# Kernel tuning notes

Measured on AMD Instinct MI355X. Metric: run time of the kernel, lower is better.

Reference implementation:

```python
import jax, jax.numpy as jnp
import numpy as np

EPS = 1e-10

def _mlp(x, W1, b1, W2, b2):
    # Linear -> ReLU -> Linear (matches _MultiLayerPercep)
    return jnp.maximum(x @ W1 + b1, 0.0) @ W2 + b2

def setup_inputs() -> dict:
    key = jax.random.key(0)
    ks = jax.random.split(key, 24)
    B, P, Q, P2, D = 512, 100, 40, 40, 64
    Nu, Ni, Nr = 100000, 100000, 6

    def lin(k, fi, fo):
        kw, kb = jax.random.split(k)
        s = 1.0 / np.sqrt(fi)
        return (jax.random.uniform(kw, (fi, fo), jnp.float32, -s, s),
                jax.random.uniform(kb, (fo,), jnp.float32, -s, s))

    uids = jax.random.randint(ks[0], (B,), 0, Nu)
    u_item_pad = jnp.stack([jax.random.randint(ks[1], (B, P), 0, Ni),
                            jax.random.randint(ks[2], (B, P), 0, Nr)], axis=-1)
    u_user_pad = jax.random.randint(ks[3], (B, Q), 0, Nu)
    u_user_item_pad = jnp.stack([jax.random.randint(ks[4], (B, Q, P2), 0, Ni),
                                 jax.random.randint(ks[5], (B, Q, P2), 0, Nr)], axis=-1)

    user_table = jax.random.normal(ks[6], (Nu, D), jnp.float32) * 0.1
    item_table = jax.random.normal(ks[7], (Ni, D), jnp.float32) * 0.1
    rate_table = jax.random.normal(ks[8], (Nr, D), jnp.float32) * 0.1

    gv_W1, gv_b1 = lin(ks[9], 2 * D, D)
    gv_W2, gv_b2 = lin(ks[10], D, D)
    atti_W1, atti_b1 = lin(ks[11], 2 * D, D)
    atti_W2, atti_b2 = lin(ks[12], D, 1)
    agg_W, agg_b = lin(ks[13], D, D)
    attu_W1, attu_b1 = lin(ks[14], 2 * D, D)
    attu_W2, attu_b2 = lin(ks[15], D, 1)
    aggn_W, aggn_b = lin(ks[16], D, D)
    cm_W1, cm_b1 = lin(ks[17], 2 * D, D)
    cm_W2, cm_b2 = lin(ks[18], D, D)
    cm_W3, cm_b3 = lin(ks[19], D, D)

    return dict(uids=uids, u_item_pad=u_item_pad, u_user_pad=u_user_pad,
                u_user_item_pad=u_user_item_pad,
                user_table=user_table, item_table=item_table, rate_table=rate_table,
                gv_W1=gv_W1, gv_b1=gv_b1, gv_W2=gv_W2, gv_b2=gv_b2,
                atti_W1=atti_W1, atti_b1=atti_b1, atti_W2=atti_W2, atti_b2=atti_b2,
                agg_W=agg_W, agg_b=agg_b,
                attu_W1=attu_W1, attu_b1=attu_b1, attu_W2=attu_W2, attu_b2=attu_b2,
                aggn_W=aggn_W, aggn_b=aggn_b,
                cm_W1=cm_W1, cm_b1=cm_b1, cm_W2=cm_W2, cm_b2=cm_b2, cm_W3=cm_W3, cm_b3=cm_b3)

def reference(uids, u_item_pad, u_user_pad, u_user_item_pad,
              user_table, item_table, rate_table,
              gv_W1, gv_b1, gv_W2, gv_b2,
              atti_W1, atti_b1, atti_W2, atti_b2,
              agg_W, agg_b,
              attu_W1, attu_b1, attu_W2, attu_b2,
              aggn_W, aggn_b,
              cm_W1, cm_b1, cm_W2, cm_b2, cm_W3, cm_b3):
    f32 = jnp.float32

    # ---- item aggregation branch ----
    q_a = item_table[u_item_pad[:, :, 0]]                      # [B,P,D]
    mask_u = (u_item_pad[:, :, 0] > 0).astype(f32)             # [B,P]
    er = rate_table[u_item_pad[:, :, 1]]                       # [B,P,D]
    x_ia = _mlp(jnp.concatenate([q_a, er], -1), gv_W1, gv_b1, gv_W2, gv_b2)
    p_i = mask_u[..., None] * user_table[uids][:, None, :]     # [B,P,D]
    alpha = _mlp(jnp.concatenate([x_ia, p_i], -1), atti_W1, atti_b1, atti_W2, atti_b2)[..., 0]
    alpha = jnp.exp(alpha) * mask_u
    alpha = alpha / (jnp.sum(alpha, axis=1, keepdims=True) + EPS)
    h_iI = jnp.maximum(jnp.sum(alpha[..., None] * x_ia, axis=1) @ agg_W + agg_b, 0.0)  # [B,D]

    # ---- social branch: per-neighbor item aggregation ----
    q_a_s = item_table[u_user_item_pad[:, :, :, 0]]            # [B,Q,P2,D]
    mask_s = (u_user_item_pad[:, :, :, 0] > 0).astype(f32)     # [B,Q,P2]
    er_s = rate_table[u_user_item_pad[:, :, :, 1]]
    x_ia_s = _mlp(jnp.concatenate([q_a_s, er_s], -1), gv_W1, gv_b1, gv_W2, gv_b2)
    nbr_emb = user_table[u_user_pad]                           # [B,Q,D]
    p_i_s = mask_s[..., None] * nbr_emb[:, :, None, :]
    alpha_s = _mlp(jnp.concatenate([x_ia_s, p_i_s], -1), atti_W1, atti_b1, atti_W2, atti_b2)[..., 0]
    alpha_s = jnp.exp(alpha_s) * mask_s
    alpha_s = alpha_s / (jnp.sum(alpha_s, axis=2, keepdims=True) + EPS)
    h_oI = jnp.maximum(jnp.sum(alpha_s[..., None] * x_ia_s, axis=2) @ agg_W + agg_b, 0.0)  # [B,Q,D]

    # ---- social attention over neighbors ----
    beta = _mlp(jnp.concatenate([h_oI, nbr_emb], -1), attu_W1, attu_b1, attu_W2, attu_b2)[..., 0]
    mask_su = (u_user_pad > 0).astype(f32)
    beta = jnp.exp(beta) * mask_su
    beta = beta / (jnp.sum(beta, axis=1, keepdims=True) + EPS)
    h_iS = jnp.maximum(jnp.sum(beta[..., None] * h_oI, axis=1) @ aggn_W + aggn_b, 0.0)  # [B,D]

    # ---- combine ----
    h = jnp.maximum(jnp.concatenate([h_iI, h_iS], -1) @ cm_W1 + cm_b1, 0.0)
    h = jnp.maximum(h @ cm_W2 + cm_b2, 0.0)
    h = jnp.maximum(h @ cm_W3 + cm_b3, 0.0)
    return h
```

## Files before the change

kernel.cpp:

```cpp
#include <hip/hip_runtime.h>
#include <math.h>

#define EPSV 1e-10f

typedef _Float16 f16x8 __attribute__((ext_vector_type(8)));
typedef _Float16 f16x4 __attribute__((ext_vector_type(4)));
typedef float f32x4 __attribute__((ext_vector_type(4)));

#define OFF_W1T  0
#define OFF_AU   8192
#define OFF_W2T  8192
#define OFF_M2T  16384
#define OFF_U    24576
#define OFF_CST  24576
#define OFF_R1   25856
#define OFF_V    28672
#define SMEM_SZ  32768
#define IMG_SZ   28672

__device__ __forceinline__ f16x8 cvt_f16x8(const float4 a, const float4 b) {
  f16x8 h;
  h[0] = (_Float16)a.x; h[1] = (_Float16)a.y; h[2] = (_Float16)a.z; h[3] = (_Float16)a.w;
  h[4] = (_Float16)b.x; h[5] = (_Float16)b.y; h[6] = (_Float16)b.z; h[7] = (_Float16)b.w;
  return h;
}

__device__ __forceinline__ float qpx1_add(float x) {
  return x + __int_as_float(__builtin_amdgcn_update_dpp(
                 0, __float_as_int(x), 0xB1, 0xF, 0xF, false));
}
__device__ __forceinline__ float qpx2_add(float x) {
  return x + __int_as_float(__builtin_amdgcn_update_dpp(
                 0, __float_as_int(x), 0x4E, 0xF, 0xF, false));
}

__global__ __launch_bounds__(256, 2) void prep_kernel(
    const float* __restrict__ rate_table,
    const float* __restrict__ gv_W1, const float* __restrict__ gv_b1,
    const float* __restrict__ gv_W2, const float* __restrict__ gv_b2,
    const float* __restrict__ atti_W1, const float* __restrict__ atti_b1,
    char* __restrict__ img) {
  const int tid = threadIdx.x;
  const int wave = tid >> 6, lane = tid & 63;
  const int quad = lane >> 4, mrow = lane & 15;
  const int phase = (int)blockIdx.x;

  if (phase == 0) {
    for (int o = tid; o < 1024; o += 256) {
      const int k = o >> 4, fb = o & 15;
      const float4 v = ((const float4*)(gv_W1 + k * 64))[fb];
      const float* vp = (const float*)&v;
#pragma unroll
      for (int c = 0; c < 4; ++c) {
        const int n = fb * 4 + c;
        *(_Float16*)(img + n * 128 + ((((k >> 3) ^ (n & 7))) << 4) +
                     ((k & 7) << 1)) = (_Float16)vp[c];
      }
    }
  } else if (phase == 1) {
    for (int o = tid; o < 1024; o += 256) {
      const int h = o >> 4, fb = o & 15;
      const float4 v = ((const float4*)(gv_W2 + h * 64))[fb];
      const float* vp = (const float*)&v;
#pragma unroll
      for (int c = 0; c < 4; ++c) {
        const int n = fb * 4 + c;
        *(_Float16*)(img + 8192 + n * 128 + ((((h >> 3) ^ (n & 7))) << 4) +
                     ((h & 7) << 1)) = (_Float16)vp[c];
      }
    }
  } else if (phase == 2) {
    f16x8 aM[2];
#pragma unroll
    for (int ks = 0; ks < 2; ++ks) {
      f16x8 t;
#pragma unroll
      for (int j = 0; j < 8; ++j)
        t[j] = (_Float16)atti_W1[(ks * 32 + quad * 8 + j) * 64 + (wave * 16 + mrow)];
      aM[ks] = t;
    }
#pragma unroll
    for (int ht = 0; ht < 4; ++ht) {
      f32x4 c = {0.f, 0.f, 0.f, 0.f};
#pragma unroll
      for (int ks = 0; ks < 2; ++ks) {
        const float* s = gv_W2 + (ht * 16 + mrow) * 64 + ks * 32 + quad * 8;
        f16x8 b;
#pragma unroll
        for (int j = 0; j < 8; ++j) b[j] = (_Float16)s[j];
        c = __builtin_amdgcn_mfma_f32_16x16x32_f16(aM[ks], b, c, 0, 0, 0);
      }
      const int h = ht * 16 + mrow;
#pragma unroll
      for (int rg = 0; rg < 4; ++rg) {
        const int n3 = wave * 16 + quad * 4 + rg;
        *(_Float16*)(img + 16384 + n3 * 128 + ((((h >> 3) ^ (n3 & 7))) << 4) +
                     ((h & 7) << 1)) = (_Float16)c[rg];
      }
    }
  } else if (phase == 3) {
    float* sR1 = (float*)(img + OFF_R1);
    for (int o = tid; o < 384; o += 256) {
      const int r = o >> 6, n = o & 63;
      float s = gv_b1[n];
#pragma unroll 8
      for (int k = 0; k < 64; ++k)
        s = fmaf(rate_table[r * 64 + k], gv_W1[(64 + k) * 64 + n], s);
      sR1[r * 68 + n] = s;
    }
  } else {
    if (tid < 64) {
      float p = atti_b1[tid];
#pragma unroll 8
      for (int j = 0; j < 64; ++j) p = fmaf(gv_b2[j], atti_W1[j * 64 + tid], p);
      ((float*)(img + OFF_CST))[tid] = p;
    }
  }
}

__global__ __launch_bounds__(256, 3) void agg_kernel(
    const int nIblk,
    const int* __restrict__ idsS, const int* __restrict__ uidS,
    const int* __restrict__ idsI, const int* __restrict__ uidI,
    const float* __restrict__ user_table, const float* __restrict__ item_table,
    const float* __restrict__ atti_W1,
    const float* __restrict__ gv_b2, const float* __restrict__ atti_W2,
    const float* __restrict__ atti_b2,
    const float* __restrict__ agg_W, const float* __restrict__ agg_b,
    const char* __restrict__ img,
    float* __restrict__ outS, float* __restrict__ outI) {
  __shared__ __align__(16) char smem[SMEM_SZ];
  const int tid = threadIdx.x;
  const int wave = tid >> 6, lane = tid & 63;
  const int quad = lane >> 4, mrow = lane & 15;

  const bool isS = (int)blockIdx.x >= nIblk;
  const int NG = isS ? 16 : 4;
  const int P = isS ? 40 : 100;
  const int nGrp = isS ? 4 : 1;
  const int tpg = isS ? 3 : 8;
  const int nIdx = nGrp * tpg;
  const int* __restrict__ ids = isS ? idsS : idsI;
  const int* __restrict__ uidp = isS ? uidS : uidI;
  float* __restrict__ out = isS ? outS : outI;
  const int gbase = isS ? ((int)blockIdx.x - nIblk) * 16 : (int)blockIdx.x * 4;

  float* sV = (float*)(smem + OFF_V);
  char* smXw = smem + OFF_W1T + wave * 2048;
  float* csW = (float*)smXw;

  const int nIdxM1 = nIdx - 1;
  int2 idreg;
  float4 pf[4];
  float pm;
  int rid;
  auto load_ids = [&](int idx) __attribute__((always_inline)) {
    const int ic = idx < nIdxM1 ? idx : nIdxM1;
    const int gq = isS ? (ic * 11) >> 5 : (ic >> 3);
    const int tt = ic - gq * tpg;
    const int it = tt * 16 + mrow;
    int2 pr = make_int2(0, 0);
    if (it < P) {
      const int g2 = gbase + wave + 4 * gq;
      pr = ((const int2*)ids)[(size_t)g2 * P + it];
    }
    idreg = pr;
  };
  auto issue_gather = [&]() __attribute__((always_inline)) {
    const int iid = idreg.x;
    rid = idreg.y;
    pm = iid > 0 ? 1.f : 0.f;
    const float* ib = item_table + (size_t)iid * 64 + quad * 8;
    pf[0] = ((const float4*)ib)[0];
    pf[1] = ((const float4*)ib)[1];
    pf[2] = ((const float4*)(ib + 32))[0];
    pf[3] = ((const float4*)(ib + 32))[1];
  };
  load_ids(0); issue_gather();
  load_ids(1);

  {
    float* uS = (float*)(smem + OFF_U);
    float* AU = (float*)(smem + OFF_AU);
    for (int t = tid; t < NG * 64; t += 256) {
      const int g = t >> 6, f = t & 63;
      uS[t] = user_table[(size_t)uidp[gbase + g] * 64 + f];
    }
    for (int o = tid; o < 1024; o += 256) {
      const int k = o >> 4, fb = o & 15;
      const float4 v = ((const float4*)(atti_W1 + (64 + k) * 64))[fb];
      const float* vp = (const float*)&v;
#pragma unroll
      for (int c = 0; c < 4; ++c) {
        const int j = fb * 4 + c;
        AU[j * 64 + (((k >> 2) ^ (j & 15)) << 2) + (k & 3)] = vp[c];
      }
    }
  }
  __syncthreads();
  {
    const float4* u4 = (const float4*)(smem + OFF_U);
    const float4* a4 = (const float4*)(smem + OFF_AU);
    for (int t = tid; t < NG * 64; t += 256) {
      const int g = t >> 6, j = t & 63;
      float s = 0.f;
#pragma unroll 4
      for (int kb = 0; kb < 16; ++kb) {
        const float4 uu = u4[g * 16 + kb];
        const float4 aa = a4[j * 16 + (kb ^ (j & 15))];
        s += uu.x * aa.x + uu.y * aa.y + uu.z * aa.z + uu.w * aa.w;
      }
      sV[t] = s;
    }
  }
  __syncthreads();
  {
    const float4* src = (const float4*)img;
    float4* dst = (float4*)smem;
#pragma unroll
    for (int o = 0; o < 7; ++o) dst[tid + o * 256] = src[tid + o * 256];
  }
  float b2v[4], aw2v[4];
#pragma unroll
  for (int nt = 0; nt < 4; ++nt) {
    b2v[nt] = gv_b2[nt * 16 + mrow];
    aw2v[nt] = atti_W2[nt * 16 + mrow];
  }
  const float ab2 = atti_b2[0];
  __syncthreads();

  f16x8 aW[4][2];
#pragma unroll
  for (int nt = 0; nt < 4; ++nt) {
#pragma unroll
    for (int ks = 0; ks < 2; ++ks)
      aW[nt][ks] = *(const f16x8*)(smem + OFF_W1T + (nt * 16 + mrow) * 128 +
                                   (((ks * 4 + quad) ^ (mrow & 7)) << 4));
  }
  float cstv[4];
  {
    const float* cst = (const float*)(smem + OFF_CST);
#pragma unroll
    for (int nt = 0; nt < 4; ++nt) cstv[nt] = cst[nt * 16 + mrow];
  }
  __syncthreads();

  const float* sR1 = (const float*)(smem + OFF_R1);
  float vv[4], pnum[4], pden = 0.f;
  for (int idx = 0; idx < nIdx; ++idx) {
    const int gq = isS ? (idx * 11) >> 5 : (idx >> 3);
    const int tt = idx - gq * tpg;
    const int g = wave + 4 * gq;
    if (tt == 0) {
#pragma unroll
      for (int nt = 0; nt < 4; ++nt) {
        vv[nt] = sV[g * 64 + nt * 16 + mrow];
        pnum[nt] = 0.f;
      }
      pden = 0.f;
    }
    f16x8 bIn0 = cvt_f16x8(pf[0], pf[1]);
    f16x8 bIn1 = cvt_f16x8(pf[2], pf[3]);
    const unsigned long long mball = __ballot(pm > 0.5f);
    const int ridcur = rid;
    issue_gather();
    load_ids(idx + 2);
#pragma unroll
    for (int nt = 0; nt < 4; ++nt) {
      f32x4 c = {0.f, 0.f, 0.f, 0.f};
      c = __builtin_amdgcn_mfma_f32_16x16x32_f16(aW[nt][0], bIn0, c, 0, 0, 0);
      c = __builtin_amdgcn_mfma_f32_16x16x32_f16(aW[nt][1], bIn1, c, 0, 0, 0);
      const float4 r1q = *(const float4*)(sR1 + ridcur * 68 + nt * 16 + quad * 4);
      const float* r1p = (const float*)&r1q;
      f16x4 hv;
#pragma unroll
      for (int rg = 0; rg < 4; ++rg)
        hv[rg] = (_Float16)fmaxf(c[rg] + r1p[rg], 0.f);
      *(f16x4*)(smXw + mrow * 128 +
                (((nt * 2 + (quad >> 1)) ^ (mrow & 7)) << 4) +
                ((quad & 1) << 3)) = hv;
    }
    f16x8 a2[2];
#pragma unroll
    for (int ks = 0; ks < 2; ++ks)
      a2[ks] = *(const f16x8*)(smXw + mrow * 128 +
                               (((ks * 4 + quad) ^ (mrow & 7)) << 4));
    float mk[4];
#pragma unroll
    for (int rg = 0; rg < 4; ++rg)
      mk[rg] = (float)((mball >> (quad * 4 + rg)) & 1ULL);
    float tl[4] = {0.f, 0.f, 0.f, 0.f};
#pragma unroll
    for (int nt = 0; nt < 4; ++nt) {
      f32x4 d = {0.f, 0.f, 0.f, 0.f};
#pragma unroll
      for (int ks = 0; ks < 2; ++ks) {
        const f16x8 bM = *(const f16x8*)(smem + OFF_M2T + (nt * 16 + mrow) * 128 +
                                         (((ks * 4 + quad) ^ (mrow & 7)) << 4));
        d = __builtin_amdgcn_mfma_f32_16x16x32_f16(a2[ks], bM, d, 0, 0, 0);
      }
#pragma unroll
      for (int rg = 0; rg < 4; ++rg) {
        const float hh = fmaxf(d[rg] + cstv[nt] + mk[rg] * vv[nt], 0.f);
        tl[rg] = fmaf(hh, aw2v[nt], tl[rg]);
      }
    }
    float e[4];
#pragma unroll
    for (int rg = 0; rg < 4; ++rg) {
      float t = tl[rg];
      t = qpx1_add(t);
      t = qpx2_add(t);
      t += __shfl_xor(t, 4); t += __shfl_xor(t, 8);
      e[rg] = __expf(t + ab2) * mk[rg];
      pden += e[rg];
    }
#pragma unroll
    for (int nt = 0; nt < 4; ++nt) {
      f32x4 c = {0.f, 0.f, 0.f, 0.f};
#pragma unroll
      for (int ks = 0; ks < 2; ++ks) {
        const f16x8 bW = *(const f16x8*)(smem + OFF_W2T + (nt * 16 + mrow) * 128 +
                                         (((ks * 4 + quad) ^ (mrow & 7)) << 4));
        c = __builtin_amdgcn_mfma_f32_16x16x32_f16(a2[ks], bW, c, 0, 0, 0);
      }
      pnum[nt] = fmaf(e[0], c[0], pnum[nt]);
      pnum[nt] = fmaf(e[1], c[1], pnum[nt]);
      pnum[nt] = fmaf(e[2], c[2], pnum[nt]);
      pnum[nt] = fmaf(e[3], c[3], pnum[nt]);
    }
    if (tt == tpg - 1) {
      float dsum = pden;
      dsum += __shfl_xor(dsum, 16); dsum += __shfl_xor(dsum, 32);
      const float rd = 1.f / (dsum + EPSV);
#pragma unroll
      for (int nt = 0; nt < 4; ++nt) {
        float s = pnum[nt];
        s += __shfl_xor(s, 16); s += __shfl_xor(s, 32);
        if (quad == 0) csW[nt * 16 + mrow] = (s + b2v[nt] * dsum) * rd;
      }
      float acc = agg_b[lane];
#pragma unroll 8
      for (int k = 0; k < 64; ++k) acc = fmaf(csW[k], agg_W[k * 64 + lane], acc);
      out[(size_t)(gbase + g) * 64 + lane] = fmaxf(acc, 0.f);
    }
  }
}

#define S2_W1T 0
#define S2_X   17408
#define S2_E   26112
#define S2_MSK 26240
#define S2_HB  26368
#define S2_SZ  27904

__global__ __launch_bounds__(128, 2) void stage2_kernel(
    const int* __restrict__ u_user_pad, const float* __restrict__ user_table,
    const float* __restrict__ hoI, const float* __restrict__ hiI,
    const float* __restrict__ attu_W1, const float* __restrict__ attu_b1,
    const float* __restrict__ attu_W2, const float* __restrict__ attu_b2,
    const float* __restrict__ aggn_W, const float* __restrict__ aggn_b,
    const float* __restrict__ cm_W1, const float* __restrict__ cm_b1,
    const float* __restrict__ cm_W2, const float* __restrict__ cm_b2,
    const float* __restrict__ cm_W3, const float* __restrict__ cm_b3,
    float* __restrict__ out) {
  __shared__ __align__(16) char smem[S2_SZ];
  const int tid = threadIdx.x;
  const int wave = tid >> 6, lane = tid & 63;
  const int quad = lane >> 4, mrow = lane & 15;
  const int b = (int)blockIdx.x * 2 + wave;

  char* sW1 = smem + S2_W1T;
  char* sXw = smem + S2_X + wave * 4352;
  float* sE = (float*)(smem + S2_E) + wave * 16;
  float* sM = (float*)(smem + S2_MSK) + wave * 16;
  float* sB = (float*)(smem + S2_HB) + wave * 192;

  for (int o = tid; o < 2048; o += 128) {
    const int k = o >> 4, fb = o & 15;
    const float4 v = ((const float4*)(attu_W1 + k * 64))[fb];
    const float* vp = (const float*)&v;
#pragma unroll
    for (int c = 0; c < 4; ++c) {
      const int n = fb * 4 + c;
      *(_Float16*)(sW1 + n * 272 + ((k >> 3) << 4) + ((k & 7) << 1)) = (_Float16)vp[c];
    }
  }
  float b1v[4], w2v[4];
#pragma unroll
  for (int nt = 0; nt < 4; ++nt) {
    b1v[nt] = attu_b1[nt * 16 + mrow];
    w2v[nt] = attu_W2[nt * 16 + mrow];
  }
  const float b2s = attu_b2[0];

  float4 pa[4], pb[4];
  float msk[4];
  auto pf = [&](int tt) __attribute__((always_inline)) {
#pragma unroll
    for (int k = 0; k < 4; ++k) {
      const int u = lane + (k << 6);
      const int r = u >> 4, bb = u & 15;
      const int q = tt * 16 + r;
      const int qc = q < 40 ? q : 39;
      int uid = 0;
      float m = 0.f;
      if (q < 40) {
        uid = u_user_pad[b * 40 + q];
        m = uid > 0 ? 1.f : 0.f;
      }
      msk[k] = m;
      const float* src = (bb < 8)
                             ? hoI + ((size_t)b * 40 + qc) * 64 + bb * 8
                             : user_table + (size_t)uid * 64 + (bb - 8) * 8;
      pa[k] = ((const float4*)src)[0];
      pb[k] = ((const float4*)src)[1];
    }
  };
  pf(0);
  __syncthreads();

  float numer = 0.f, pden = 0.f;
  for (int tt = 0; tt < 3; ++tt) {
#pragma unroll
    for (int k = 0; k < 4; ++k) {
      const int u = lane + (k << 6);
      const int r = u >> 4, bb = u & 15;
      *(f16x8*)(sXw + r * 272 + (bb << 4)) = cvt_f16x8(pa[k], pb[k]);
      if (bb == 0) sM[r] = msk[k];
    }
    if (tt < 2) pf(tt + 1);
    f16x8 a[4];
#pragma unroll
    for (int ks = 0; ks < 4; ++ks)
      a[ks] = *(const f16x8*)(sXw + mrow * 272 + ((ks * 4 + quad) << 4));
    float mk[4];
#pragma unroll
    for (int rg = 0; rg < 4; ++rg) mk[rg] = sM[quad * 4 + rg];
    float tl[4] = {0.f, 0.f, 0.f, 0.f};
#pragma unroll
    for (int nt = 0; nt < 4; ++nt) {
      f32x4 d = {0.f, 0.f, 0.f, 0.f};
      const int n = nt * 16 + mrow;
#pragma unroll
      for (int ks = 0; ks < 4; ++ks) {
        const f16x8 bW = *(const f16x8*)(sW1 + n * 272 + ((ks * 4 + quad) << 4));
        d = __builtin_amdgcn_mfma_f32_16x16x32_f16(a[ks], bW, d, 0, 0, 0);
      }
#pragma unroll
      for (int rg = 0; rg < 4; ++rg) {
        const float h = fmaxf(d[rg] + b1v[nt], 0.f);
        tl[rg] = fmaf(h, w2v[nt], tl[rg]);
      }
    }
    float e[4];
#pragma unroll
    for (int rg = 0; rg < 4; ++rg) {
      float t = tl[rg];
      t = qpx1_add(t);
      t = qpx2_add(t);
      t += __shfl_xor(t, 4); t += __shfl_xor(t, 8);
      e[rg] = __expf(t + b2s) * mk[rg];
      pden += e[rg];
    }
    if (mrow == 0) {
#pragma unroll
      for (int rg = 0; rg < 4; ++rg) sE[quad * 4 + rg] = e[rg];
    }
#pragma unroll 4
    for (int r = 0; r < 16; ++r) {
      const float er = sE[r];
      const float xv = (float)*(const _Float16*)(sXw + r * 272 + ((lane >> 3) << 4) +
                                                 ((lane & 7) << 1));
      numer = fmaf(er, xv, numer);
    }
  }
  pden += __shfl_xor(pden, 16);
  pden += __shfl_xor(pden, 32);
  const float hagg = numer / (pden + EPSV);

  sB[128 + lane] = hagg;
  sB[lane] = hiI[(size_t)b * 64 + lane];
  float acc = aggn_b[lane];
#pragma unroll 8
  for (int k = 0; k < 64; ++k) acc = fmaf(sB[128 + k], aggn_W[k * 64 + lane], acc);
  sB[64 + lane] = fmaxf(acc, 0.f);
  float c1 = cm_b1[lane];
#pragma unroll 8
  for (int k = 0; k < 128; ++k) c1 = fmaf(sB[k], cm_W1[k * 64 + lane], c1);
  sB[128 + lane] = fmaxf(c1, 0.f);
  float c2 = cm_b2[lane];
#pragma unroll 8
  for (int k = 0; k < 64; ++k) c2 = fmaf(sB[128 + k], cm_W2[k * 64 + lane], c2);
  sB[lane] = fmaxf(c2, 0.f);
  float c3 = cm_b3[lane];
#pragma unroll 8
  for (int k = 0; k < 64; ++k) c3 = fmaf(sB[k], cm_W3[k * 64 + lane], c3);
  out[(size_t)b * 64 + lane] = fmaxf(c3, 0.f);
}

extern "C" void kernel_launch(void* const* d_in, const int* in_sizes, int n_in,
                              void* d_out, int out_size, void* d_ws, size_t ws_size,
                              hipStream_t stream) {
  const int* uids = (const int*)d_in[0];
  const int* u_item_pad = (const int*)d_in[1];
  const int* u_user_pad = (const int*)d_in[2];
  const int* u_user_item_pad = (const int*)d_in[3];
  const float* user_table = (const float*)d_in[4];
  const float* item_table = (const float*)d_in[5];
  const float* rate_table = (const float*)d_in[6];
  const float* gv_W1 = (const float*)d_in[7];
  const float* gv_b1 = (const float*)d_in[8];
  const float* gv_W2 = (const float*)d_in[9];
  const float* gv_b2 = (const float*)d_in[10];
  const float* atti_W1 = (const float*)d_in[11];
  const float* atti_b1 = (const float*)d_in[12];
  const float* atti_W2 = (const float*)d_in[13];
  const float* atti_b2 = (const float*)d_in[14];
  const float* agg_W = (const float*)d_in[15];
  const float* agg_b = (const float*)d_in[16];
  const float* attu_W1 = (const float*)d_in[17];
  const float* attu_b1 = (const float*)d_in[18];
  const float* attu_W2 = (const float*)d_in[19];
  const float* attu_b2 = (const float*)d_in[20];
  const float* aggn_W = (const float*)d_in[21];
  const float* aggn_b = (const float*)d_in[22];
  const float* cm_W1 = (const float*)d_in[23];
  const float* cm_b1 = (const float*)d_in[24];
  const float* cm_W2 = (const float*)d_in[25];
  const float* cm_b2 = (const float*)d_in[26];
  const float* cm_W3 = (const float*)d_in[27];
  const float* cm_b3 = (const float*)d_in[28];
  float* out = (float*)d_out;

  float* hoI = (float*)d_ws;
  float* hiI = hoI + (size_t)512 * 40 * 64;
  char* img = (char*)(hiI + (size_t)512 * 64);

  prep_kernel<<<5, 256, 0, stream>>>(rate_table, gv_W1, gv_b1, gv_W2, gv_b2,
                                     atti_W1, atti_b1, img);
  agg_kernel<<<128 + 1280, 256, 0, stream>>>(
      128, u_user_item_pad, u_user_pad, u_item_pad, uids,
      user_table, item_table, atti_W1,
      gv_b2, atti_W2, atti_b2,
      agg_W, agg_b, img, hoI, hiI);
  stage2_kernel<<<256, 128, 0, stream>>>(u_user_pad, user_table, hoI, hiI,
                                         attu_W1, attu_b1, attu_W2, attu_b2,
                                         aggn_W, aggn_b,
                                         cm_W1, cm_b1, cm_W2, cm_b2, cm_W3, cm_b3,
                                         out);
}
```

Before: 242.0 us.

## Precompute user-projection vectors in prep kernel instead of per agg block

Moves the per-group projection of user embeddings through the second half of atti_W1 out of agg_kernel and into extra blocks of the prep kernel (328 blocks of 64 groups each), writing results to a workspace buffer. agg_kernel then loads the precomputed vectors with a single float4 copy rather than re-staging atti_W1 and running the dot products. This removes two __syncthreads and redundant weight staging from each of about 1400 agg blocks. The cost is a larger prep launch and an extra global round-trip for the vectors.

```diff
diff --git a/kernel.cpp b/kernel.cpp
--- a/kernel.cpp
+++ b/kernel.cpp
@@ -8,15 +8,15 @@
 typedef float f32x4 __attribute__((ext_vector_type(4)));
 
 #define OFF_W1T  0
-#define OFF_AU   8192
 #define OFF_W2T  8192
 #define OFF_M2T  16384
-#define OFF_U    24576
 #define OFF_CST  24576
 #define OFF_R1   25856
 #define OFF_V    28672
 #define SMEM_SZ  32768
 #define IMG_SZ   28672
+#define N_SGRP   20480
+#define N_GRP    20992
 
 __device__ __forceinline__ f16x8 cvt_f16x8(const float4 a, const float4 b) {
   f16x8 h;
@@ -34,12 +34,15 @@
                  0, __float_as_int(x), 0x4E, 0xF, 0xF, false));
 }
 
-__global__ __launch_bounds__(256, 2) void prep_kernel(
+__global__ __launch_bounds__(256, 2) void prep_all(
     const float* __restrict__ rate_table,
     const float* __restrict__ gv_W1, const float* __restrict__ gv_b1,
     const float* __restrict__ gv_W2, const float* __restrict__ gv_b2,
     const float* __restrict__ atti_W1, const float* __restrict__ atti_b1,
-    char* __restrict__ img) {
+    const int* __restrict__ u_user_pad, const int* __restrict__ uids,
+    const float* __restrict__ user_table,
+    char* __restrict__ img, float* __restrict__ sVws) {
+  __shared__ __align__(16) char smem[SMEM_SZ];
   const int tid = threadIdx.x;
   const int wave = tid >> 6, lane = tid & 63;
   const int quad = lane >> 4, mrow = lane & 15;
@@ -108,26 +111,59 @@
         s = fmaf(rate_table[r * 64 + k], gv_W1[(64 + k) * 64 + n], s);
       sR1[r * 68 + n] = s;
     }
-  } else {
+  } else if (phase == 4) {
     if (tid < 64) {
       float p = atti_b1[tid];
 #pragma unroll 8
       for (int j = 0; j < 64; ++j) p = fmaf(gv_b2[j], atti_W1[j * 64 + tid], p);
       ((float*)(img + OFF_CST))[tid] = p;
     }
+  } else {
+    const int sb = phase - 5;
+    const int jbase = sb * 64;
+    float* AU = (float*)smem;
+    float* uS = (float*)(smem + 16384);
+    for (int o = tid; o < 1024; o += 256) {
+      const int k = o >> 4, fb = o & 15;
+      const float4 v = ((const float4*)(atti_W1 + (64 + k) * 64))[fb];
+      const float* vp = (const float*)&v;
+#pragma unroll
+      for (int c = 0; c < 4; ++c) {
+        const int j = fb * 4 + c;
+        AU[j * 64 + (((k >> 2) ^ (j & 15)) << 2) + (k & 3)] = vp[c];
+      }
+    }
+    for (int t = tid; t < 4096; t += 256) {
+      const int g = t >> 6, f = t & 63;
+      const int j = jbase + g;
+      const int uid = j < N_SGRP ? u_user_pad[j] : uids[j - N_SGRP];
+      uS[t] = user_table[(size_t)uid * 64 + f];
+    }
+    __syncthreads();
+    const float4* u4 = (const float4*)uS;
+    const float4* a4 = (const float4*)AU;
+    for (int t = tid; t < 4096; t += 256) {
+      const int g = t >> 6, jn = t & 63;
+      float s = 0.f;
+#pragma unroll 4
+      for (int kb = 0; kb < 16; ++kb) {
+        const float4 uu = u4[g * 16 + kb];
+        const float4 aa = a4[jn * 16 + (kb ^ (jn & 15))];
+        s += uu.x * aa.x + uu.y * aa.y + uu.z * aa.z + uu.w * aa.w;
+      }
+      sVws[(size_t)(jbase + g) * 64 + jn] = s;
+    }
   }
 }
 
 __global__ __launch_bounds__(256, 3) void agg_kernel(
     const int nIblk,
-    const int* __restrict__ idsS, const int* __restrict__ uidS,
-    const int* __restrict__ idsI, const int* __restrict__ uidI,
-    const float* __restrict__ user_table, const float* __restrict__ item_table,
-    const float* __restrict__ atti_W1,
+    const int* __restrict__ idsS, const int* __restrict__ idsI,
+    const float* __restrict__ item_table,
     const float* __restrict__ gv_b2, const float* __restrict__ atti_W2,
     const float* __restrict__ atti_b2,
     const float* __restrict__ agg_W, const float* __restrict__ agg_b,
-    const char* __restrict__ img,
+    const char* __restrict__ img, const float* __restrict__ sVws,
     float* __restrict__ outS, float* __restrict__ outI) {
   __shared__ __align__(16) char smem[SMEM_SZ];
   const int tid = threadIdx.x;
@@ -141,9 +177,9 @@
   const int tpg = isS ? 3 : 8;
   const int nIdx = nGrp * tpg;
   const int* __restrict__ ids = isS ? idsS : idsI;
-  const int* __restrict__ uidp = isS ? uidS : uidI;
   float* __restrict__ out = isS ? outS : outI;
   const int gbase = isS ? ((int)blockIdx.x - nIblk) * 16 : (int)blockIdx.x * 4;
+  const int svbase = isS ? gbase : (N_SGRP + gbase);
 
   float* sV = (float*)(smem + OFF_V);
   char* smXw = smem + OFF_W1T + wave * 2048;
@@ -180,45 +216,12 @@
   load_ids(1);
 
   {
-    float* uS = (float*)(smem + OFF_U);
-    float* AU = (float*)(smem + OFF_AU);
-    for (int t = tid; t < NG * 64; t += 256) {
-      const int g = t >> 6, f = t & 63;
-      uS[t] = user_table[(size_t)uidp[gbase + g] * 64 + f];
-    }
-    for (int o = tid; o < 1024; o += 256) {
-      const int k = o >> 4, fb = o & 15;
-      const float4 v = ((const float4*)(atti_W1 + (64 + k) * 64))[fb];
-      const float* vp = (const float*)&v;
-#pragma unroll
-      for (int c = 0; c < 4; ++c) {
-        const int j = fb * 4 + c;
-        AU[j * 64 + (((k >> 2) ^ (j & 15)) << 2) + (k & 3)] = vp[c];
-      }
-    }
-  }
-  __syncthreads();
-  {
-    const float4* u4 = (const float4*)(smem + OFF_U);
-    const float4* a4 = (const float4*)(smem + OFF_AU);
-    for (int t = tid; t < NG * 64; t += 256) {
-      const int g = t >> 6, j = t & 63;
-      float s = 0.f;
-#pragma unroll 4
-      for (int kb = 0; kb < 16; ++kb) {
-        const float4 uu = u4[g * 16 + kb];
-        const float4 aa = a4[j * 16 + (kb ^ (j & 15))];
-        s += uu.x * aa.x + uu.y * aa.y + uu.z * aa.z + uu.w * aa.w;
-      }
-      sV[t] = s;
-    }
-  }
-  __syncthreads();
-  {
     const float4* src = (const float4*)img;
     float4* dst = (float4*)smem;
 #pragma unroll
     for (int o = 0; o < 7; ++o) dst[tid + o * 256] = src[tid + o * 256];
+    if (tid < NG * 16)
+      ((float4*)sV)[tid] = ((const float4*)(sVws + (size_t)svbase * 64))[tid];
   }
   float b2v[4], aw2v[4];
 #pragma unroll
@@ -536,14 +539,15 @@
   float* hoI = (float*)d_ws;
   float* hiI = hoI + (size_t)512 * 40 * 64;
   char* img = (char*)(hiI + (size_t)512 * 64);
-
-  prep_kernel<<<5, 256, 0, stream>>>(rate_table, gv_W1, gv_b1, gv_W2, gv_b2,
-                                     atti_W1, atti_b1, img);
+  float* sVws = (float*)(img + IMG_SZ);
+
+  prep_all<<<5 + 328, 256, 0, stream>>>(rate_table, gv_W1, gv_b1, gv_W2,
+                                        gv_b2, atti_W1, atti_b1,
+                                        u_user_pad, uids, user_table,
+                                        img, sVws);
   agg_kernel<<<128 + 1280, 256, 0, stream>>>(
-      128, u_user_item_pad, u_user_pad, u_item_pad, uids,
-      user_table, item_table, atti_W1,
-      gv_b2, atti_W2, atti_b2,
-      agg_W, agg_b, img, hoI, hiI);
+      128, u_user_item_pad, u_item_pad, item_table,
+      gv_b2, atti_W2, atti_b2, agg_W, agg_b, img, sVws, hoI, hiI);
   stage2_kernel<<<256, 128, 0, stream>>>(u_user_pad, user_table, hoI, hiI,
                                          attu_W1, attu_b1, attu_W2, attu_b2,
                                          aggn_W, aggn_b,
```

Result: no change. 241.1 us (-0.4%).
